# Kernel optimization log

Hardware: AMD Instinct MI355X
Metric: run time of the kernel (lower is better)

Reference implementation:

```python
import jax, jax.numpy as jnp
import numpy as np

HIDDEN = 2048
N_HEADS = 16
N_KV_HEADS = 8
HEAD_DIM = 128  # == head_dim_original, no padding needed
ROPE_THETA = 1000000.0
EPS = 1e-6
T_NOISE = 512
T_CTX = 1536
MAX_KV = 8192


def rms_norm(x, scale, eps=EPS):
    # normalize over last axis (head_dim), per-head like nnx.RMSNorm(head_dim)
    var = jnp.mean(x * x, axis=-1, keepdims=True)
    return x * jax.lax.rsqrt(var + eps) * scale


def apply_rope(x, positions, head_dim=HEAD_DIM, theta=ROPE_THETA):
    # x: (T, N, H), positions: (T,) int
    inv_freq = 1.0 / (theta ** (jnp.arange(0, head_dim, 2, dtype=jnp.float32) / head_dim))
    ang = positions.astype(jnp.float32)[:, None] * inv_freq  # (T, H/2)
    cos = jnp.cos(ang)[:, None, :]  # (T, 1, H/2)
    sin = jnp.sin(ang)[:, None, :]
    x1, x2 = jnp.split(x, 2, axis=-1)
    return jnp.concatenate([x1 * cos - x2 * sin, x2 * cos + x1 * sin], axis=-1).astype(x.dtype)


def setup_inputs() -> dict:
    key = jax.random.key(0)
    ks = jax.random.split(key, 10)
    s = 0.02
    return {
        "x_noise": jax.random.normal(ks[0], (T_NOISE, HIDDEN), jnp.float32),
        "target_hidden": jax.random.normal(ks[1], (T_CTX, HIDDEN), jnp.float32),
        "noise_positions": jnp.arange(T_NOISE, dtype=jnp.int32) + T_CTX,
        "ctx_positions": jnp.arange(T_CTX, dtype=jnp.int32),
        "kv_cache_k": jax.random.normal(ks[2], (1, N_HEADS, MAX_KV, HEAD_DIM), jnp.float32),
        "kv_cache_v": jax.random.normal(ks[3], (1, N_HEADS, MAX_KV, HEAD_DIM), jnp.float32),
        "cache_len": 2048,
        "wq": jax.random.normal(ks[4], (HIDDEN, N_HEADS, HEAD_DIM), jnp.float32) * s,
        "wk": jax.random.normal(ks[5], (HIDDEN, N_KV_HEADS, HEAD_DIM), jnp.float32) * s,
        "wv": jax.random.normal(ks[6], (HIDDEN, N_KV_HEADS, HEAD_DIM), jnp.float32) * s,
        "wo": jax.random.normal(ks[7], (N_HEADS, HEAD_DIM, HIDDEN), jnp.float32) * s,
        "q_scale": jnp.ones((HEAD_DIM,), jnp.float32) + jax.random.uniform(ks[8], (HEAD_DIM,), jnp.float32, -0.05, 0.05),
        "k_scale": jnp.ones((HEAD_DIM,), jnp.float32) + jax.random.uniform(ks[9], (HEAD_DIM,), jnp.float32, -0.05, 0.05),
    }


def reference(x_noise, target_hidden, noise_positions, ctx_positions, kv_cache_k,
              kv_cache_v, cache_len, wq, wk, wv, wo, q_scale, k_scale):
    num_kv_groups = N_HEADS // N_KV_HEADS
    t_noise = x_noise.shape[0]

    # 1. Q projection + RMSNorm + RoPE
    q = jnp.einsum('td,dnh->tnh', x_noise, wq)
    q = rms_norm(q, q_scale)
    q = apply_rope(q, noise_positions)

    # 2. K/V over [context, noise]
    x_new = jnp.concatenate([target_hidden, x_noise], axis=0)  # (T_new, D)
    k_new = jnp.einsum('td,dkh->tkh', x_new, wk)
    v_new = jnp.einsum('td,dkh->tkh', x_new, wv)
    k_new = rms_norm(k_new, k_scale)
    new_positions = jnp.concatenate([ctx_positions, noise_positions], axis=0)
    k_new = apply_rope(k_new, new_positions)

    # 3. GQA head repeat
    if num_kv_groups > 1:
        k_new = jnp.repeat(k_new, num_kv_groups, axis=1)
        v_new = jnp.repeat(v_new, num_kv_groups, axis=1)

    # 4. Scatter new K/V into cache at dynamic offset cache_len
    t_new = x_new.shape[0]
    k_new_4d = k_new.transpose(1, 0, 2)[None]  # (1, N, T_new, H)
    v_new_4d = v_new.transpose(1, 0, 2)[None]
    kv_cache_k = jax.lax.dynamic_update_slice(kv_cache_k, k_new_4d, (0, 0, cache_len, 0))
    kv_cache_v = jax.lax.dynamic_update_slice(kv_cache_v, v_new_4d, (0, 0, cache_len, 0))
    new_cache_len = cache_len + t_new
    max_kv = kv_cache_k.shape[2]

    # 5. Non-causal attention over valid cache (segment-id mask = valid length)
    q_4d = q.transpose(1, 0, 2)[None]  # (1, N, T_noise, H)
    sm_scale = HEAD_DIM ** -0.5
    scores = jnp.einsum('bnth,bnsh->bnts', q_4d, kv_cache_k) * sm_scale  # (1,N,Tq,S)
    valid = jnp.arange(max_kv) < new_cache_len  # (S,)
    scores = jnp.where(valid[None, None, None, :], scores, jnp.float32(-1e30))
    probs = jax.nn.softmax(scores, axis=-1)
    attn = jnp.einsum('bnts,bnsh->bnth', probs, kv_cache_v)
    attn = attn[0].transpose(1, 0, 2)  # (T_noise, N, H)

    output = jnp.einsum('tnh,nhd->td', attn, wo)
    return output, kv_cache_k, kv_cache_v
```

## Files before the change

kernel.cpp:

```cpp
#include <hip/hip_runtime.h>
#include <hip/hip_bf16.h>

#define HIDDEN 2048
#define NH 16
#define NKV 8
#define HD 128
#define TN 512
#define TC 1536
#define TNEW 2048
#define MAXKV 8192

using u16 = unsigned short;
using u32 = unsigned int;

typedef short short8 __attribute__((ext_vector_type(8)));
typedef float floatx4 __attribute__((ext_vector_type(4)));

__device__ __forceinline__ u16 f2bf(float f) {
  u32 u = __float_as_uint(f);
  u += 0x7FFFu + ((u >> 16) & 1u);
  return (u16)(u >> 16);
}

__device__ __forceinline__ uint4 pack8(const float* f) {
  uint4 r;
  r.x = (u32)f2bf(f[0]) | ((u32)f2bf(f[1]) << 16);
  r.y = (u32)f2bf(f[2]) | ((u32)f2bf(f[3]) << 16);
  r.z = (u32)f2bf(f[4]) | ((u32)f2bf(f[5]) << 16);
  r.w = (u32)f2bf(f[6]) | ((u32)f2bf(f[7]) << 16);
  return r;
}

__device__ __forceinline__ short8 ldfrag(const u16* p) {
  uint4 v = *(const uint4*)p;
  return __builtin_bit_cast(short8, v);
}

__device__ __forceinline__ void gload16(const void* g, void* l) {
  __builtin_amdgcn_global_load_lds(
      (const __attribute__((address_space(1))) u32*)g,
      (__attribute__((address_space(3))) u32*)l, 16, 0, 0);
}

__global__ __launch_bounds__(256) void conv_bf16(
    const float4* __restrict__ in, uint2* __restrict__ out, int n4)
{
  int idx = blockIdx.x * 256 + threadIdx.x;
  if (idx >= n4) return;
  float4 v = in[idx];
  uint2 r;
  r.x = (u32)f2bf(v.x) | ((u32)f2bf(v.y) << 16);
  r.y = (u32)f2bf(v.z) | ((u32)f2bf(v.w) << 16);
  out[idx] = r;
}

__global__ __launch_bounds__(256) void transpose_bf16(
    const float* __restrict__ w, u16* __restrict__ wT, int K, int N)
{
  __shared__ float t[64][65];
  const int bk = blockIdx.y * 64, bn = blockIdx.x * 64;
  const int tid = threadIdx.x;
  const int r = tid >> 4, c4 = (tid & 15) * 4;
#pragma unroll
  for (int rr = 0; rr < 4; rr++) {
    float4 v = *(const float4*)(w + (size_t)(bk + rr * 16 + r) * N + bn + c4);
    t[rr * 16 + r][c4 + 0] = v.x;
    t[rr * 16 + r][c4 + 1] = v.y;
    t[rr * 16 + r][c4 + 2] = v.z;
    t[rr * 16 + r][c4 + 3] = v.w;
  }
  __syncthreads();
  const int n = tid >> 2, k16 = (tid & 3) * 16;
  u32 wbuf[8];
#pragma unroll
  for (int jj = 0; jj < 8; jj++) {
    float lo = t[k16 + 2 * jj][n], hi = t[k16 + 2 * jj + 1][n];
    wbuf[jj] = (u32)f2bf(lo) | ((u32)f2bf(hi) << 16);
  }
  *(uint4*)(&wT[(size_t)(bn + n) * K + bk + k16])     = *(uint4*)(wbuf);
  *(uint4*)(&wT[(size_t)(bn + n) * K + bk + k16 + 8]) = *(uint4*)(wbuf + 4);
}

__global__ __launch_bounds__(256) void vT_build(
    const float* __restrict__ inV, const float* __restrict__ vproj,
    const int* __restrict__ clp, u16* __restrict__ VbT)
{
  __shared__ float t[64][65];
  const int cl = *clp;
  const int s0 = blockIdx.x * 64;
  const int slim = cl + TNEW;
  if (s0 >= slim) return;
  const int h0 = blockIdx.y * 64;
  const int head = blockIdx.z;
  const int tid = threadIdx.x;

  const int rr = tid >> 2, c16 = (tid & 3) * 16;
  int s = s0 + rr;
  if (s >= slim) s = slim - 1;
  const float* src = (s < cl)
      ? inV + ((size_t)head * MAXKV + s) * HD + (h0 + c16)
      : vproj + (size_t)(s - cl) * (NKV * HD) + (head >> 1) * HD + (h0 + c16);
  float4 v0 = ((const float4*)src)[0];
  float4 v1 = ((const float4*)src)[1];
  float4 v2 = ((const float4*)src)[2];
  float4 v3 = ((const float4*)src)[3];
  *(float4*)&t[rr][c16 + 0]  = v0;
  *(float4*)&t[rr][c16 + 4]  = v1;
  *(float4*)&t[rr][c16 + 8]  = v2;
  *(float4*)&t[rr][c16 + 12] = v3;
  __syncthreads();

  const int hh = tid >> 2, sseg = (tid & 3) * 16;
  u32 wbuf[8];
#pragma unroll
  for (int j = 0; j < 8; j++)
    wbuf[j] = (u32)f2bf(t[sseg + 2 * j][hh]) | ((u32)f2bf(t[sseg + 2 * j + 1][hh]) << 16);
  u16* dst = VbT + ((size_t)head * HD + h0 + hh) * MAXKV + s0 + sseg;
  *(uint4*)(dst)     = *(uint4*)(wbuf);
  *(uint4*)(dst + 8) = *(uint4*)(wbuf + 4);
}

__global__ __launch_bounds__(256) void cache_copy(
    const float4* __restrict__ inK, const float4* __restrict__ inV,
    float4* __restrict__ outK, float4* __restrict__ outV,
    const int* __restrict__ clp, u16* __restrict__ Kb)
{
  const int cl = *clp;
  long long idx = (long long)blockIdx.x * 256 + threadIdx.x;
  const long long per = (long long)NH * MAXKV * (HD / 4);
  const float4* src; float4* dst; bool isv;
  long long r = idx;
  if (r < per) { src = inK; dst = outK; isv = false; }
  else { r -= per; src = inV; dst = outV; isv = true; }
  int row = (int)((r >> 5) & (MAXKV - 1));
  if (row >= cl && row < cl + TNEW) return;
  float4 v = src[r];
  dst[r] = v;
  if (!isv && row < cl && Kb) {
    uint2 p;
    p.x = (u32)f2bf(v.x) | ((u32)f2bf(v.y) << 16);
    p.y = (u32)f2bf(v.z) | ((u32)f2bf(v.w) << 16);
    *(uint2*)(Kb + (size_t)r * 4) = p;
  }
}

__global__ __launch_bounds__(256) void gemm_v2(
    const u16* __restrict__ A0, int rows0, const u16* __restrict__ A1,
    const u16* __restrict__ B0, const u16* __restrict__ B1, int Nhalf,
    float* __restrict__ C0, float* __restrict__ C1,
    int M, int N, int K, int ksteps)
{
  __shared__ u16 As[2][128 * 32];
  __shared__ u16 Bs[2][128 * 32];
  const int tid = threadIdx.x;
  const int lane = tid & 63, wave = tid >> 6;
  const int quad = lane >> 4, m16 = lane & 15;

  const int gx = gridDim.x, gy = gridDim.y;
  int bx = blockIdx.x, by = blockIdx.y;
  if (((gx & 3) == 0) && ((gy & 1) == 0)) {
    const int lin = bx + gx * by;
    const int c = lin & 7, j = lin >> 3;
    const int sw = gx >> 2, sh = gy >> 1;
    bx = (c & 3) * sw + j % sw;
    by = (c >> 2) * sh + j / sw;
  }
  const int bm = by * 128, bn = bx * 128;
  const int wm = (wave >> 1) * 64, wn = (wave & 1) * 64;
  const int z = blockIdx.z;
  const int kbase = z * ksteps * 32;

  const u16* B = (bn < Nhalf) ? B0 : B1;
  float*     C = (bn < Nhalf) ? C0 : C1;
  const int n0 = (bn < Nhalf) ? bn : bn - Nhalf;
  const int strideN = (bn < Nhalf) ? Nhalf : (N - Nhalf);

  floatx4 acc[4][4];
#pragma unroll
  for (int i = 0; i < 4; i++)
#pragma unroll
    for (int j = 0; j < 4; j++)
#pragma unroll
      for (int r = 0; r < 4; r++) acc[i][j][r] = 0.0f;

  const int srow = tid >> 2;
  const int sk = (tid & 3) * 8;
  const int ar0 = bm + srow, ar1 = bm + srow + 64;
  const u16* Arow0 = (ar0 < rows0) ? (A0 + (size_t)ar0 * K)
                                   : (A1 + (size_t)(ar0 - rows0) * K);
  const u16* Arow1 = (ar1 < rows0) ? (A0 + (size_t)ar1 * K)
                                   : (A1 + (size_t)(ar1 - rows0) * K);
  const u16* Brow0 = B + (size_t)(n0 + srow) * K;
  const u16* Brow1 = B + (size_t)(n0 + srow + 64) * K;
  const int wb = wave * 512;

  {
    const int k0 = kbase;
    gload16(Arow0 + k0 + sk, &As[0][wb]);
    gload16(Arow1 + k0 + sk, &As[0][2048 + wb]);
    gload16(Brow0 + k0 + sk, &Bs[0][wb]);
    gload16(Brow1 + k0 + sk, &Bs[0][2048 + wb]);
  }
  int b = 0;
  for (int ks = 0; ks < ksteps; ks++) {
    if (ks + 1 < ksteps) {
      const int k1 = kbase + (ks + 1) * 32;
      gload16(Arow0 + k1 + sk, &As[b ^ 1][wb]);
      gload16(Arow1 + k1 + sk, &As[b ^ 1][2048 + wb]);
      gload16(Brow0 + k1 + sk, &Bs[b ^ 1][wb]);
      gload16(Brow1 + k1 + sk, &Bs[b ^ 1][2048 + wb]);
      asm volatile("s_waitcnt vmcnt(4)" ::: "memory");
    } else {
      asm volatile("s_waitcnt vmcnt(0)" ::: "memory");
    }
    __builtin_amdgcn_s_barrier();
    __builtin_amdgcn_sched_barrier(0);

    short8 af[4], bfr[4];
#pragma unroll
    for (int i = 0; i < 4; i++) {
      af[i]  = ldfrag(&As[b][(wm + i * 16 + m16) * 32 + quad * 8]);
      bfr[i] = ldfrag(&Bs[b][(wn + i * 16 + m16) * 32 + quad * 8]);
    }
#pragma unroll
    for (int i = 0; i < 4; i++)
#pragma unroll
      for (int j = 0; j < 4; j++)
        acc[i][j] = __builtin_amdgcn_mfma_f32_16x16x32_bf16(af[i], bfr[j], acc[i][j], 0, 0, 0);

    asm volatile("s_waitcnt lgkmcnt(0)" ::: "memory");
    __builtin_amdgcn_s_barrier();
    __builtin_amdgcn_sched_barrier(0);
    b ^= 1;
  }

  const size_t zoff = (size_t)z * M * Nhalf;
#pragma unroll
  for (int i = 0; i < 4; i++)
#pragma unroll
    for (int j = 0; j < 4; j++)
#pragma unroll
      for (int r = 0; r < 4; r++) {
        int row = bm + wm + i * 16 + quad * 4 + r;
        int col = wn + j * 16 + m16;
        C[zoff + (size_t)row * strideN + n0 + col] = acc[i][j][r];
      }
}

__global__ __launch_bounds__(256) void gemm_bf16(
    const float* __restrict__ A0, int rows0, const float* __restrict__ A1,
    const float* __restrict__ B0, const float* __restrict__ B1, int Nhalf,
    float* __restrict__ C0, float* __restrict__ C1,
    int M, int N, int K, int ksteps)
{
  __shared__ u16 As[64 * 40];
  __shared__ u16 Bs[64 * 40];
  const int tid = threadIdx.x;
  const int lane = tid & 63;
  const int wave = tid >> 6;
  const int quad = lane >> 4;
  const int m16 = lane & 15;
  const int bm = blockIdx.y * 64;
  const int bn = blockIdx.x * 64;
  const int wm = (wave >> 1) * 32;
  const int wn = (wave & 1) * 32;
  const int z = blockIdx.z;
  const int kbase = z * ksteps * 32;

  const float* B = (bn < Nhalf) ? B0 : B1;
  float*       C = (bn < Nhalf) ? C0 : C1;
  const int n0 = (bn < Nhalf) ? bn : bn - Nhalf;
  const int strideN = (bn < Nhalf) ? Nhalf : (N - Nhalf);

  floatx4 acc[2][2];
#pragma unroll
  for (int i = 0; i < 2; i++)
#pragma unroll
    for (int j = 0; j < 2; j++)
#pragma unroll
      for (int r = 0; r < 4; r++) acc[i][j][r] = 0.0f;

  const int arow = tid >> 2, akg = (tid & 3) * 8;
  const int brow = tid >> 3, bng = (tid & 7) * 8;
  const int garow = bm + arow;
  const float* Ap = (garow < rows0) ? (A0 + (size_t)garow * K)
                                    : (A1 + (size_t)(garow - rows0) * K);

  for (int ks = 0; ks < ksteps; ks++) {
    const int k0 = kbase + ks * 32;
    if (k0 >= K) break;
    float av[8];
    *(float4*)(av)     = *(const float4*)(Ap + k0 + akg);
    *(float4*)(av + 4) = *(const float4*)(Ap + k0 + akg + 4);
    *(uint4*)&As[arow * 40 + akg] = pack8(av);

    float bv[8];
    const float* Bp = B + (size_t)(k0 + brow) * strideN + n0 + bng;
    *(float4*)(bv)     = *(const float4*)(Bp);
    *(float4*)(bv + 4) = *(const float4*)(Bp + 4);
#pragma unroll
    for (int j = 0; j < 8; j++) Bs[(bng + j) * 40 + brow] = f2bf(bv[j]);

    __syncthreads();

    short8 a0 = ldfrag(&As[(wm + m16) * 40 + quad * 8]);
    short8 a1 = ldfrag(&As[(wm + 16 + m16) * 40 + quad * 8]);
    short8 b0 = ldfrag(&Bs[(wn + m16) * 40 + quad * 8]);
    short8 b1 = ldfrag(&Bs[(wn + 16 + m16) * 40 + quad * 8]);
    acc[0][0] = __builtin_amdgcn_mfma_f32_16x16x32_bf16(a0, b0, acc[0][0], 0, 0, 0);
    acc[0][1] = __builtin_amdgcn_mfma_f32_16x16x32_bf16(a0, b1, acc[0][1], 0, 0, 0);
    acc[1][0] = __builtin_amdgcn_mfma_f32_16x16x32_bf16(a1, b0, acc[1][0], 0, 0, 0);
    acc[1][1] = __builtin_amdgcn_mfma_f32_16x16x32_bf16(a1, b1, acc[1][1], 0, 0, 0);

    __syncthreads();
  }

  const size_t zoff = (size_t)z * M * Nhalf;
#pragma unroll
  for (int mt = 0; mt < 2; mt++)
#pragma unroll
    for (int nt = 0; nt < 2; nt++)
#pragma unroll
      for (int r = 0; r < 4; r++) {
        int row = bm + wm + mt * 16 + quad * 4 + r;
        int col = wn + nt * 16 + m16;
        C[zoff + (size_t)row * strideN + n0 + col] = acc[mt][nt][r];
      }
}

__global__ __launch_bounds__(256) void reduce4(
    const float4* __restrict__ P, float4* __restrict__ C, int n4)
{
  int idx = blockIdx.x * 256 + threadIdx.x;
  if (idx >= n4) return;
  float4 a = P[idx], b = P[idx + n4], c = P[idx + 2 * n4], d = P[idx + 3 * n4];
  float4 r;
  r.x = (a.x + b.x) + (c.x + d.x);
  r.y = (a.y + b.y) + (c.y + d.y);
  r.z = (a.z + b.z) + (c.z + d.z);
  r.w = (a.w + b.w) + (c.w + d.w);
  C[idx] = r;
}

__global__ __launch_bounds__(64) void q_post_k(
    const float* __restrict__ qproj, const int* __restrict__ npos,
    const float* __restrict__ qscale, u16* __restrict__ qbf)
{
  const int t = blockIdx.x, n = blockIdx.y, i = threadIdx.x;
  const size_t base = (size_t)t * HIDDEN + n * HD;
  const float x1 = qproj[base + i];
  const float x2 = qproj[base + i + 64];
  float ss = x1 * x1 + x2 * x2;
#pragma unroll
  for (int m = 1; m < 64; m <<= 1) ss += __shfl_xor(ss, m, 64);
  const float rstd = rsqrtf(ss * (1.0f / HD) + 1e-6f);
  float y1 = x1 * rstd * qscale[i];
  float y2 = x2 * rstd * qscale[i + 64];
  const float pos = (float)npos[t];
  const float ang = pos * exp2f(-(float)i * (19.931568569324174f / 64.0f));
  const float c = cosf(ang), s = sinf(ang);
  const float sc = 0.08838834764831845f * 1.4426950408889634f;
  qbf[base + i]      = f2bf((y1 * c - y2 * s) * sc);
  qbf[base + i + 64] = f2bf((y2 * c + y1 * s) * sc);
}

__global__ __launch_bounds__(64) void k_post_k(
    const float* __restrict__ kproj, const int* __restrict__ ctxpos,
    const int* __restrict__ npos, const float* __restrict__ kscale,
    const int* __restrict__ clp, float* __restrict__ outK, u16* __restrict__ Kb)
{
  const int t = blockIdx.x, kh = blockIdx.y, i = threadIdx.x;
  const int cl = *clp;
  const size_t base = (size_t)t * (NKV * HD) + kh * HD;
  const float x1 = kproj[base + i];
  const float x2 = kproj[base + i + 64];
  float ss = x1 * x1 + x2 * x2;
#pragma unroll
  for (int m = 1; m < 64; m <<= 1) ss += __shfl_xor(ss, m, 64);
  const float rstd = rsqrtf(ss * (1.0f / HD) + 1e-6f);
  float y1 = x1 * rstd * kscale[i];
  float y2 = x2 * rstd * kscale[i + 64];
  const int posi = (t < TC) ? ctxpos[t] : npos[t - TC];
  const float ang = (float)posi * exp2f(-(float)i * (19.931568569324174f / 64.0f));
  const float c = cosf(ang), s = sinf(ang);
  const float o1 = y1 * c - y2 * s;
  const float o2 = y2 * c + y1 * s;
  const size_t row = (size_t)cl + t;
  const size_t b0 = ((size_t)(2 * kh) * MAXKV + row) * HD;
  const size_t b1 = ((size_t)(2 * kh + 1) * MAXKV + row) * HD;
  outK[b0 + i] = o1; outK[b0 + i + 64] = o2;
  outK[b1 + i] = o1; outK[b1 + i + 64] = o2;
  if (Kb) {
    const u16 s1 = f2bf(o1), s2 = f2bf(o2);
    Kb[b0 + i] = s1; Kb[b0 + i + 64] = s2;
    Kb[b1 + i] = s1; Kb[b1 + i + 64] = s2;
  }
}

__global__ __launch_bounds__(128) void v_post_k(
    const float* __restrict__ vproj, const int* __restrict__ clp,
    float* __restrict__ outV)
{
  const int t = blockIdx.x, kh = blockIdx.y, h = threadIdx.x;
  const int cl = *clp;
  const float v = vproj[(size_t)t * (NKV * HD) + kh * HD + h];
  const size_t row = (size_t)cl + t;
  outV[((size_t)(2 * kh) * MAXKV + row) * HD + h] = v;
  outV[((size_t)(2 * kh + 1) * MAXKV + row) * HD + h] = v;
}

__global__ __launch_bounds__(256) void attn_sh(
    const u16* __restrict__ qbf, const u16* __restrict__ Kb,
    const u16* __restrict__ VbT, const int* __restrict__ clp,
    float* __restrict__ Opart, float* __restrict__ Oml, int splits)
{
  __shared__ u16 Ks[2][32 * 128];
  __shared__ u16 Vt[2][128 * 32];
  __shared__ u16 Ps[4][16 * 40];

  const int tid = threadIdx.x;
  const int lane = tid & 63, wave = tid >> 6;
  const int quad = lane >> 4, m16 = lane & 15;

  const int lin = blockIdx.x;
  const int ppx = (NH * splits) >> 3;
  const int c = lin & 7;
  const int jj = lin >> 3;
  const int pair = c * ppx + (jj % ppx);
  const int x = jj / ppx;
  const int head = pair & (NH - 1);
  const int z = pair >> 4;

  const int qbase = x * 64 + wave * 16;
  const int Svalid = *clp + TNEW;
  const int ntiles = (Svalid + 31) >> 5;
  const int per = (ntiles + splits - 1) / splits;
  const int it0 = z * per;
  const int it1 = (ntiles < it0 + per) ? ntiles : (it0 + per);

  short8 qf[4];
#pragma unroll
  for (int kb = 0; kb < 4; kb++)
    qf[kb] = ldfrag(&qbf[((size_t)(qbase + m16) * NH + head) * HD + kb * 32 + quad * 8]);

  floatx4 O[8];
#pragma unroll
  for (int i = 0; i < 8; i++)
#pragma unroll
    for (int r = 0; r < 4; r++) O[i][r] = 0.0f;
  float lrow[4];
#pragma unroll
  for (int r = 0; r < 4; r++) lrow[r] = 0.0f;

  const int krow = tid >> 4;
  const int ksrccol = ((tid & 15) * 16) ^ ((krow & 7) << 4);
  const char* Kbase = (const char*)(Kb + (size_t)head * MAXKV * HD);
  const int vh = tid >> 2;
  const int vs8 = (tid & 3) * 8;
  const char* Vbase = (const char*)(VbT + (size_t)head * HD * MAXKV);
  u16* myPs = &Ps[wave][0];
  const int kxor = (m16 & 7) << 4;
  const int wb = wave * 512;

  int b = 0;
  if (it0 < it1) {
    {
      const int s0 = it0 * 32;
      gload16(Kbase + ((size_t)(s0 + krow) << 8) + ksrccol,          &Ks[0][wb]);
      gload16(Kbase + ((size_t)(s0 + krow + 16) << 8) + ksrccol,     &Ks[0][2048 + wb]);
      gload16(Vbase + (((size_t)vh * MAXKV + s0 + vs8) << 1),        &Vt[0][wb]);
      gload16(Vbase + (((size_t)(vh + 64) * MAXKV + s0 + vs8) << 1), &Vt[0][2048 + wb]);
    }
    for (int it = it0; it < it1; ++it) {
      if (it + 1 < it1) {
        const int s1 = (it + 1) * 32;
        u16* KsN = &Ks[b ^ 1][0];
        u16* VtN = &Vt[b ^ 1][0];
        gload16(Kbase + ((size_t)(s1 + krow) << 8) + ksrccol,          KsN + wb);
        gload16(Kbase + ((size_t)(s1 + krow + 16) << 8) + ksrccol,     KsN + 2048 + wb);
        gload16(Vbase + (((size_t)vh * MAXKV + s1 + vs8) << 1),        VtN + wb);
        gload16(Vbase + (((size_t)(vh + 64) * MAXKV + s1 + vs8) << 1), VtN + 2048 + wb);
        asm volatile("s_waitcnt vmcnt(4) lgkmcnt(0)" ::: "memory");
      } else {
        asm volatile("s_waitcnt vmcnt(0) lgkmcnt(0)" ::: "memory");
      }
      __builtin_amdgcn_s_barrier();
      __builtin_amdgcn_sched_barrier(0);

      const u16* KsB = &Ks[b][0];
      const u16* VtB = &Vt[b][0];
      const int s0 = it * 32;

      floatx4 sc[2];
#pragma unroll
      for (int st = 0; st < 2; st++) {
        floatx4 a;
#pragma unroll
        for (int r = 0; r < 4; r++) a[r] = 0.0f;
        const int rofs = (st * 16 + m16) * 128;
#pragma unroll
        for (int kb = 0; kb < 4; kb++) {
          short8 kf = ldfrag(&KsB[rofs + (((kb * 64 + quad * 16) ^ kxor) >> 1)]);
          a = __builtin_amdgcn_mfma_f32_16x16x32_bf16(qf[kb], kf, a, 0, 0, 0);
        }
        const int scol = s0 + st * 16 + m16;
        if (scol >= Svalid) {
#pragma unroll
          for (int r = 0; r < 4; r++) a[r] = -1e30f;
        }
        sc[st] = a;
      }

#pragma unroll
      for (int st = 0; st < 2; st++)
#pragma unroll
        for (int r = 0; r < 4; r++) sc[st][r] = exp2f(sc[st][r]);
#pragma unroll
      for (int r = 0; r < 4; r++) lrow[r] += sc[0][r] + sc[1][r];

#pragma unroll
      for (int st = 0; st < 2; st++)
#pragma unroll
        for (int r = 0; r < 4; r++)
          myPs[(quad * 4 + r) * 40 + st * 16 + m16] = f2bf(sc[st][r]);
      short8 pfr = ldfrag(&myPs[m16 * 40 + quad * 8]);
#pragma unroll
      for (int hb = 0; hb < 8; hb++) {
        short8 vf = ldfrag(&VtB[(hb * 16 + m16) * 32 + quad * 8]);
        O[hb] = __builtin_amdgcn_mfma_f32_16x16x32_bf16(pfr, vf, O[hb], 0, 0, 0);
      }

      asm volatile("s_waitcnt lgkmcnt(0)" ::: "memory");
      __builtin_amdgcn_s_barrier();
      __builtin_amdgcn_sched_barrier(0);
      b ^= 1;
    }
  }

#pragma unroll
  for (int r = 0; r < 4; r++) {
    lrow[r] += __shfl_xor(lrow[r], 1, 64);
    lrow[r] += __shfl_xor(lrow[r], 2, 64);
    lrow[r] += __shfl_xor(lrow[r], 4, 64);
    lrow[r] += __shfl_xor(lrow[r], 8, 64);
  }

  const size_t zbase = (size_t)z * TN * NH;
  const int trow = qbase + quad * 4;
#pragma unroll
  for (int hb = 0; hb < 8; hb++)
#pragma unroll
    for (int r = 0; r < 4; r++)
      Opart[(zbase + (size_t)(trow + r) * NH + head) * HD + hb * 16 + m16] = O[hb][r];
  if (m16 == 0) {
#pragma unroll
    for (int r = 0; r < 4; r++) {
      Oml[(zbase + (size_t)(trow + r) * NH + head) * 2 + 0] = 0.0f;
      Oml[(zbase + (size_t)(trow + r) * NH + head) * 2 + 1] = lrow[r];
    }
  }
}

__global__ __launch_bounds__(256) void attn_k(
    const u16* __restrict__ qbf, const float* __restrict__ outK,
    const float* __restrict__ outV, const int* __restrict__ clp,
    float* __restrict__ Opart, float* __restrict__ Oml)
{
  __shared__ u16 Ksl[32 * 136];
  __shared__ u16 Vtl[128 * 40];
  __shared__ u16 Psl[4 * 16 * 40];
  const int tid = threadIdx.x;
  const int lane = tid & 63, wave = tid >> 6;
  const int quad = lane >> 4, m16 = lane & 15;
  const int head = blockIdx.y;
  const int qbase = blockIdx.x * 64 + wave * 16;
  const int z = blockIdx.z, splits = gridDim.z;
  const int Svalid = *clp + TNEW;
  const int ntiles = (Svalid + 31) >> 5;
  const int per = (ntiles + splits - 1) / splits;
  const int it0 = z * per;
  const int it1 = min(ntiles, it0 + per);

  short8 qf[4];
#pragma unroll
  for (int kb = 0; kb < 4; kb++)
    qf[kb] = ldfrag(&qbf[((size_t)(qbase + m16) * NH + head) * HD + kb * 32 + quad * 8]);

  floatx4 O[8];
#pragma unroll
  for (int i = 0; i < 8; i++)
#pragma unroll
    for (int r = 0; r < 4; r++) O[i][r] = 0.0f;
  float mrow[4], lrow[4];
#pragma unroll
  for (int r = 0; r < 4; r++) { mrow[r] = -1e30f; lrow[r] = 0.0f; }

  const int sstage = tid >> 3;
  const int hg = (tid & 7) * 16;

  for (int it = it0; it < it1; it++) {
    const int s0 = it * 32;
    {
      int srow = s0 + sstage; if (srow > MAXKV - 1) srow = MAXKV - 1;
      const float* kp = outK + ((size_t)head * MAXKV + srow) * HD + hg;
      float tv[16];
      *(float4*)(tv)      = *(const float4*)(kp);
      *(float4*)(tv + 4)  = *(const float4*)(kp + 4);
      *(float4*)(tv + 8)  = *(const float4*)(kp + 8);
      *(float4*)(tv + 12) = *(const float4*)(kp + 12);
      *(uint4*)&Ksl[sstage * 136 + hg]     = pack8(tv);
      *(uint4*)&Ksl[sstage * 136 + hg + 8] = pack8(tv + 8);
      const float* vp = outV + ((size_t)head * MAXKV + srow) * HD + hg;
      float vv[16];
      *(float4*)(vv)      = *(const float4*)(vp);
      *(float4*)(vv + 4)  = *(const float4*)(vp + 4);
      *(float4*)(vv + 8)  = *(const float4*)(vp + 8);
      *(float4*)(vv + 12) = *(const float4*)(vp + 12);
#pragma unroll
      for (int j = 0; j < 16; j++) Vtl[(hg + j) * 40 + sstage] = f2bf(vv[j]);
    }
    __syncthreads();

    floatx4 sc[2];
#pragma unroll
    for (int st = 0; st < 2; st++) {
      floatx4 a;
#pragma unroll
      for (int r = 0; r < 4; r++) a[r] = 0.0f;
#pragma unroll
      for (int kb = 0; kb < 4; kb++) {
        short8 kf = ldfrag(&Ksl[(st * 16 + m16) * 136 + kb * 32 + quad * 8]);
        a = __builtin_amdgcn_mfma_f32_16x16x32_bf16(qf[kb], kf, a, 0, 0, 0);
      }
      const int scol = s0 + st * 16 + m16;
      if (scol >= Svalid) {
#pragma unroll
        for (int r = 0; r < 4; r++) a[r] = -1e30f;
      }
      sc[st] = a;
    }

    float alpha[4];
#pragma unroll
    for (int r = 0; r < 4; r++) {
      float mx = fmaxf(sc[0][r], sc[1][r]);
      mx = fmaxf(mx, __shfl_xor(mx, 1, 64));
      mx = fmaxf(mx, __shfl_xor(mx, 2, 64));
      mx = fmaxf(mx, __shfl_xor(mx, 4, 64));
      mx = fmaxf(mx, __shfl_xor(mx, 8, 64));
      const float mn = fmaxf(mrow[r], mx);
      alpha[r] = exp2f(mrow[r] - mn);
      const float p0 = exp2f(sc[0][r] - mn);
      const float p1 = exp2f(sc[1][r] - mn);
      sc[0][r] = p0; sc[1][r] = p1;
      float rs = p0 + p1;
      rs += __shfl_xor(rs, 1, 64);
      rs += __shfl_xor(rs, 2, 64);
      rs += __shfl_xor(rs, 4, 64);
      rs += __shfl_xor(rs, 8, 64);
      lrow[r] = lrow[r] * alpha[r] + rs;
      mrow[r] = mn;
    }
#pragma unroll
    for (int hb = 0; hb < 8; hb++)
#pragma unroll
      for (int r = 0; r < 4; r++) O[hb][r] *= alpha[r];

    u16* myPs = &Psl[wave * 640];
#pragma unroll
    for (int st = 0; st < 2; st++)
#pragma unroll
      for (int r = 0; r < 4; r++)
        myPs[(quad * 4 + r) * 40 + st * 16 + m16] = f2bf(sc[st][r]);
    short8 pf = ldfrag(&myPs[m16 * 40 + quad * 8]);
#pragma unroll
    for (int hb = 0; hb < 8; hb++) {
      short8 vf = ldfrag(&Vtl[(hb * 16 + m16) * 40 + quad * 8]);
      O[hb] = __builtin_amdgcn_mfma_f32_16x16x32_bf16(pf, vf, O[hb], 0, 0, 0);
    }
    __syncthreads();
  }

  const size_t zbase = (size_t)z * TN * NH;
  const int trow = qbase + quad * 4;
#pragma unroll
  for (int hb = 0; hb < 8; hb++)
#pragma unroll
    for (int r = 0; r < 4; r++)
      Opart[(zbase + (size_t)(trow + r) * NH + head) * HD + hb * 16 + m16] = O[hb][r];
  if (m16 == 0) {
#pragma unroll
    for (int r = 0; r < 4; r++) {
      Oml[(zbase + (size_t)(trow + r) * NH + head) * 2 + 0] = mrow[r];
      Oml[(zbase + (size_t)(trow + r) * NH + head) * 2 + 1] = lrow[r];
    }
  }
}

__global__ __launch_bounds__(128) void attn_combine(
    const float* __restrict__ Opart, const float* __restrict__ Oml,
    float* __restrict__ attnb, u16* __restrict__ attnbf, int splits)
{
  const int pair = blockIdx.x;
  const int h = threadIdx.x;
  float M = -1e30f;
  for (int zz = 0; zz < splits; zz++)
    M = fmaxf(M, Oml[((size_t)zz * TN * NH + pair) * 2]);
  float l = 0.0f, o = 0.0f;
  for (int zz = 0; zz < splits; zz++) {
    const float mi = Oml[((size_t)zz * TN * NH + pair) * 2];
    const float li = Oml[((size_t)zz * TN * NH + pair) * 2 + 1];
    const float w = exp2f(mi - M);
    l += li * w;
    o += Opart[((size_t)zz * TN * NH + pair) * HD + h] * w;
  }
  const float res = o / l;
  attnb[(size_t)pair * HD + h] = res;
  if (attnbf) attnbf[(size_t)pair * HD + h] = f2bf(res);
}

extern "C" void kernel_launch(void* const* d_in, const int* in_sizes, int n_in,
                              void* d_out, int out_size, void* d_ws, size_t ws_size,
                              hipStream_t stream) {
  const float* x_noise       = (const float*)d_in[0];
  const float* target_hidden = (const float*)d_in[1];
  const int*   noise_pos     = (const int*)d_in[2];
  const int*   ctx_pos       = (const int*)d_in[3];
  const float* inK           = (const float*)d_in[4];
  const float* inV           = (const float*)d_in[5];
  const int*   cache_len     = (const int*)d_in[6];
  const float* wq            = (const float*)d_in[7];
  const float* wk            = (const float*)d_in[8];
  const float* wv            = (const float*)d_in[9];
  const float* wo            = (const float*)d_in[10];
  const float* q_scale       = (const float*)d_in[11];
  const float* k_scale       = (const float*)d_in[12];

  float* out0 = (float*)d_out;
  float* outK = out0 + (size_t)TN * HIDDEN;
  float* outV = outK + (size_t)NH * MAXKV * HD;

  size_t off = 0;
  auto walloc = [&](size_t bytes) -> void* {
    void* p = (char*)d_ws + off;
    off += (bytes + 255) & ~(size_t)255;
    return p;
  };
  u16*   qbf    = (u16*)walloc((size_t)TN * HIDDEN * 2);
  float* attnb  = (float*)walloc((size_t)TN * HIDDEN * 4);
  u16*   attnbf = (u16*)walloc((size_t)TN * HIDDEN * 2);
  float* qproj  = (float*)walloc((size_t)TN * HIDDEN * 4);
  float* kproj  = (float*)walloc((size_t)TNEW * NKV * HD * 4);
  float* vproj  = (float*)walloc((size_t)TNEW * NKV * HD * 4);

  const size_t PER_SPLIT = (size_t)TN * NH * HD * 4 + (size_t)TN * NH * 8;
  const size_t SHB   = (size_t)NH * MAXKV * HD * sizeof(u16);
  const size_t GPART = (size_t)4 * TN * HIDDEN * 4;
  const size_t CONVB = ((size_t)TN * HIDDEN + (size_t)TC * HIDDEN) * 2
                     + ((size_t)HIDDEN * HIDDEN * 2
                      + (size_t)HIDDEN * (NKV * HD) * 2) * 2;
  auto maxsz = [](size_t a, size_t b) { return a > b ? a : b; };

  size_t avail = (ws_size > off) ? ws_size - off : 0;
  bool conv = false;
  int asplits = 0;
  if (avail >= CONVB + 2 * SHB + maxsz(8 * PER_SPLIT, GPART))      { conv = true; asplits = 8; }
  else if (avail >= CONVB + 2 * SHB + maxsz(4 * PER_SPLIT, GPART)) { conv = true; asplits = 4; }
  else if (avail >= 2 * SHB + maxsz(8 * PER_SPLIT, GPART))         { asplits = 8; }
  else if (avail >= 2 * SHB + maxsz(4 * PER_SPLIT, GPART))         { asplits = 4; }
  const bool shadow = (asplits > 0);

  u16 *xbf = nullptr, *thbf = nullptr, *wqT = nullptr, *wkT = nullptr,
      *wvT = nullptr, *woT = nullptr;
  if (conv) {
    xbf  = (u16*)walloc((size_t)TN * HIDDEN * 2);
    thbf = (u16*)walloc((size_t)TC * HIDDEN * 2);
    wqT  = (u16*)walloc((size_t)HIDDEN * HIDDEN * 2);
    wkT  = (u16*)walloc((size_t)HIDDEN * (NKV * HD) * 2);
    wvT  = (u16*)walloc((size_t)HIDDEN * (NKV * HD) * 2);
    woT  = (u16*)walloc((size_t)HIDDEN * HIDDEN * 2);
  }
  u16 *Kb = nullptr, *VbT = nullptr;
  if (shadow) {
    Kb  = (u16*)walloc(SHB);
    VbT = (u16*)walloc(SHB);
  }

  float* scratch = (float*)((char*)d_ws + off);
  const size_t avail2 = (ws_size > off) ? ws_size - off : 0;
  if (!shadow) {
    asplits = 2;
    if (avail2 >= 8 * PER_SPLIT) asplits = 8;
    else if (avail2 >= 4 * PER_SPLIT) asplits = 4;
  }
  float* Opart = scratch;
  float* Oml   = Opart + (size_t)asplits * TN * NH * HD;
  const bool ksplit = (avail2 >= GPART);
  float* gpart = scratch;

  if (conv) {
    conv_bf16<<<dim3((TN * HIDDEN / 4 + 255) / 256), dim3(256), 0, stream>>>(
        (const float4*)x_noise, (uint2*)xbf, TN * HIDDEN / 4);
    conv_bf16<<<dim3((TC * HIDDEN / 4 + 255) / 256), dim3(256), 0, stream>>>(
        (const float4*)target_hidden, (uint2*)thbf, TC * HIDDEN / 4);
    transpose_bf16<<<dim3(HIDDEN / 64, HIDDEN / 64), dim3(256), 0, stream>>>(
        wq, wqT, HIDDEN, HIDDEN);
    transpose_bf16<<<dim3(NKV * HD / 64, HIDDEN / 64), dim3(256), 0, stream>>>(
        wk, wkT, HIDDEN, NKV * HD);
    transpose_bf16<<<dim3(NKV * HD / 64, HIDDEN / 64), dim3(256), 0, stream>>>(
        wv, wvT, HIDDEN, NKV * HD);
    transpose_bf16<<<dim3(HIDDEN / 64, HIDDEN / 64), dim3(256), 0, stream>>>(
        wo, woT, NH * HD, HIDDEN);
  }

  cache_copy<<<dim3(32768), dim3(256), 0, stream>>>(
      (const float4*)inK, (const float4*)inV, (float4*)outK, (float4*)outV,
      cache_len, Kb);

  if (conv && ksplit) {
    gemm_v2<<<dim3(HIDDEN / 128, TN / 128, 4), dim3(256), 0, stream>>>(
        xbf, TN, xbf, wqT, wqT, HIDDEN, gpart, gpart, TN, HIDDEN, HIDDEN, 16);
    reduce4<<<dim3((TN * HIDDEN / 4 + 255) / 256), dim3(256), 0, stream>>>(
        (const float4*)gpart, (float4*)qproj, TN * HIDDEN / 4);
  } else if (conv) {
    gemm_v2<<<dim3(HIDDEN / 128, TN / 128, 1), dim3(256), 0, stream>>>(
        xbf, TN, xbf, wqT, wqT, HIDDEN, qproj, qproj, TN, HIDDEN, HIDDEN, 64);
  } else if (ksplit) {
    gemm_bf16<<<dim3(HIDDEN / 64, TN / 64, 4), dim3(256), 0, stream>>>(
        x_noise, TN, x_noise, wq, wq, HIDDEN, gpart, gpart, TN, HIDDEN, HIDDEN, 16);
    reduce4<<<dim3((TN * HIDDEN / 4 + 255) / 256), dim3(256), 0, stream>>>(
        (const float4*)gpart, (float4*)qproj, TN * HIDDEN / 4);
  } else {
    gemm_bf16<<<dim3(HIDDEN / 64, TN / 64, 1), dim3(256), 0, stream>>>(
        x_noise, TN, x_noise, wq, wq, HIDDEN, qproj, qproj, TN, HIDDEN, HIDDEN, 64);
  }

  if (conv) {
    gemm_v2<<<dim3(2 * NKV * HD / 128, TNEW / 128, 1), dim3(256), 0, stream>>>(
        thbf, TC, xbf, wkT, wvT, NKV * HD, kproj, vproj,
        TNEW, 2 * NKV * HD, HIDDEN, 64);
  } else {
    gemm_bf16<<<dim3(2 * NKV * HD / 64, TNEW / 64, 1), dim3(256), 0, stream>>>(
        target_hidden, TC, x_noise, wk, wv, NKV * HD, kproj, vproj,
        TNEW, 2 * NKV * HD, HIDDEN, 64);
  }

  q_post_k<<<dim3(TN, NH), dim3(64), 0, stream>>>(qproj, noise_pos, q_scale, qbf);
  k_post_k<<<dim3(TNEW, NKV), dim3(64), 0, stream>>>(
      kproj, ctx_pos, noise_pos, k_scale, cache_len, outK, Kb);
  v_post_k<<<dim3(TNEW, NKV), dim3(128), 0, stream>>>(vproj, cache_len, outV);
  if (shadow) {
    vT_build<<<dim3(MAXKV / 64, HD / 64, NH), dim3(256), 0, stream>>>(
        inV, vproj, cache_len, VbT);
  }

  if (shadow) {
    attn_sh<<<dim3((TN / 64) * NH * asplits), dim3(256), 0, stream>>>(
        qbf, Kb, VbT, cache_len, Opart, Oml, asplits);
  } else {
    attn_k<<<dim3(TN / 64, NH, asplits), dim3(256), 0, stream>>>(
        qbf, outK, outV, cache_len, Opart, Oml);
  }
  attn_combine<<<dim3(TN * NH), dim3(128), 0, stream>>>(
      Opart, Oml, attnb, conv ? attnbf : nullptr, asplits);

  if (conv && ksplit) {
    gemm_v2<<<dim3(HIDDEN / 128, TN / 128, 4), dim3(256), 0, stream>>>(
        attnbf, TN, attnbf, woT, woT, HIDDEN, gpart, gpart, TN, HIDDEN, HIDDEN, 16);
    reduce4<<<dim3((TN * HIDDEN / 4 + 255) / 256), dim3(256), 0, stream>>>(
        (const float4*)gpart, (float4*)out0, TN * HIDDEN / 4);
  } else if (conv) {
    gemm_v2<<<dim3(HIDDEN / 128, TN / 128, 1), dim3(256), 0, stream>>>(
        attnbf, TN, attnbf, woT, woT, HIDDEN, out0, out0, TN, HIDDEN, HIDDEN, 64);
  } else if (ksplit) {
    gemm_bf16<<<dim3(HIDDEN / 64, TN / 64, 4), dim3(256), 0, stream>>>(
        attnb, TN, attnb, wo, wo, HIDDEN, gpart, gpart, TN, HIDDEN, HIDDEN, 16);
    reduce4<<<dim3((TN * HIDDEN / 4 + 255) / 256), dim3(256), 0, stream>>>(
        (const float4*)gpart, (float4*)out0, TN * HIDDEN / 4);
  } else {
    gemm_bf16<<<dim3(HIDDEN / 64, TN / 64, 1), dim3(256), 0, stream>>>(
        attnb, TN, attnb, wo, wo, HIDDEN, out0, out0, TN, HIDDEN, HIDDEN, 64);
  }
}
```

Measured before the change: 469.7 us.

## Shrink gemm_v2 M tile to 64 and XOR-swizzle LDS fragments

The gemm_v2 block tile goes from 128x128 to 64x128, so each wave computes 32x64 and the grids double along M. This gives more blocks for the small GEMMs. It also applies an XOR swizzle to the K column within the 32-wide LDS rows for the A/B tiles in gemm_v2 and for the V tile in the attention kernel, to reduce LDS bank conflicts on fragment reads. The cost is lower arithmetic intensity per block and more global traffic for B.

```diff
diff --git a/kernel.cpp b/kernel.cpp
--- a/kernel.cpp
+++ b/kernel.cpp
@@ -150,7 +150,7 @@
     float* __restrict__ C0, float* __restrict__ C1,
     int M, int N, int K, int ksteps)
 {
-  __shared__ u16 As[2][128 * 32];
+  __shared__ u16 As[2][64 * 32];
   __shared__ u16 Bs[2][128 * 32];
   const int tid = threadIdx.x;
   const int lane = tid & 63, wave = tid >> 6;
@@ -165,8 +165,8 @@
     bx = (c & 3) * sw + j % sw;
     by = (c >> 2) * sh + j / sw;
   }
-  const int bm = by * 128, bn = bx * 128;
-  const int wm = (wave >> 1) * 64, wn = (wave & 1) * 64;
+  const int bm = by * 64, bn = bx * 128;
+  const int wm = (wave >> 1) * 32, wn = (wave & 1) * 64;
   const int z = blockIdx.z;
   const int kbase = z * ksteps * 32;
 
@@ -175,55 +175,53 @@
   const int n0 = (bn < Nhalf) ? bn : bn - Nhalf;
   const int strideN = (bn < Nhalf) ? Nhalf : (N - Nhalf);
 
-  floatx4 acc[4][4];
-#pragma unroll
-  for (int i = 0; i < 4; i++)
+  floatx4 acc[2][4];
+#pragma unroll
+  for (int i = 0; i < 2; i++)
 #pragma unroll
     for (int j = 0; j < 4; j++)
 #pragma unroll
       for (int r = 0; r < 4; r++) acc[i][j][r] = 0.0f;
 
   const int srow = tid >> 2;
-  const int sk = (tid & 3) * 8;
-  const int ar0 = bm + srow, ar1 = bm + srow + 64;
-  const u16* Arow0 = (ar0 < rows0) ? (A0 + (size_t)ar0 * K)
-                                   : (A1 + (size_t)(ar0 - rows0) * K);
-  const u16* Arow1 = (ar1 < rows0) ? (A0 + (size_t)ar1 * K)
-                                   : (A1 + (size_t)(ar1 - rows0) * K);
+  const int sk = ((tid & 3) * 8) ^ (((srow >> 1) & 3) << 3);
+  const int ar = bm + srow;
+  const u16* Arow = (ar < rows0) ? (A0 + (size_t)ar * K)
+                                 : (A1 + (size_t)(ar - rows0) * K);
   const u16* Brow0 = B + (size_t)(n0 + srow) * K;
   const u16* Brow1 = B + (size_t)(n0 + srow + 64) * K;
   const int wb = wave * 512;
 
   {
     const int k0 = kbase;
-    gload16(Arow0 + k0 + sk, &As[0][wb]);
-    gload16(Arow1 + k0 + sk, &As[0][2048 + wb]);
+    gload16(Arow  + k0 + sk, &As[0][wb]);
     gload16(Brow0 + k0 + sk, &Bs[0][wb]);
     gload16(Brow1 + k0 + sk, &Bs[0][2048 + wb]);
   }
+  const int rq = (quad * 8) ^ (((m16 >> 1) & 3) << 3);
   int b = 0;
   for (int ks = 0; ks < ksteps; ks++) {
     if (ks + 1 < ksteps) {
       const int k1 = kbase + (ks + 1) * 32;
-      gload16(Arow0 + k1 + sk, &As[b ^ 1][wb]);
-      gload16(Arow1 + k1 + sk, &As[b ^ 1][2048 + wb]);
+      gload16(Arow  + k1 + sk, &As[b ^ 1][wb]);
       gload16(Brow0 + k1 + sk, &Bs[b ^ 1][wb]);
       gload16(Brow1 + k1 + sk, &Bs[b ^ 1][2048 + wb]);
-      asm volatile("s_waitcnt vmcnt(4)" ::: "memory");
+      asm volatile("s_waitcnt vmcnt(3)" ::: "memory");
     } else {
       asm volatile("s_waitcnt vmcnt(0)" ::: "memory");
     }
     __builtin_amdgcn_s_barrier();
     __builtin_amdgcn_sched_barrier(0);
 
-    short8 af[4], bfr[4];
-#pragma unroll
-    for (int i = 0; i < 4; i++) {
-      af[i]  = ldfrag(&As[b][(wm + i * 16 + m16) * 32 + quad * 8]);
-      bfr[i] = ldfrag(&Bs[b][(wn + i * 16 + m16) * 32 + quad * 8]);
-    }
-#pragma unroll
-    for (int i = 0; i < 4; i++)
+    short8 af[2], bfr[4];
+#pragma unroll
+    for (int i = 0; i < 2; i++)
+      af[i] = ldfrag(&As[b][(wm + i * 16 + m16) * 32 + rq]);
+#pragma unroll
+    for (int j = 0; j < 4; j++)
+      bfr[j] = ldfrag(&Bs[b][(wn + j * 16 + m16) * 32 + rq]);
+#pragma unroll
+    for (int i = 0; i < 2; i++)
 #pragma unroll
       for (int j = 0; j < 4; j++)
         acc[i][j] = __builtin_amdgcn_mfma_f32_16x16x32_bf16(af[i], bfr[j], acc[i][j], 0, 0, 0);
@@ -236,7 +234,7 @@
 
   const size_t zoff = (size_t)z * M * Nhalf;
 #pragma unroll
-  for (int i = 0; i < 4; i++)
+  for (int i = 0; i < 2; i++)
 #pragma unroll
     for (int j = 0; j < 4; j++)
 #pragma unroll
@@ -456,10 +454,11 @@
   const int ksrccol = ((tid & 15) * 16) ^ ((krow & 7) << 4);
   const char* Kbase = (const char*)(Kb + (size_t)head * MAXKV * HD);
   const int vh = tid >> 2;
-  const int vs8 = (tid & 3) * 8;
+  const int vs8 = ((tid & 3) * 8) ^ (((vh >> 1) & 3) << 3);
   const char* Vbase = (const char*)(VbT + (size_t)head * HD * MAXKV);
   u16* myPs = &Ps[wave][0];
   const int kxor = (m16 & 7) << 4;
+  const int vq = (quad * 8) ^ (((m16 >> 1) & 3) << 3);
   const int wb = wave * 512;
 
   int b = 0;
@@ -526,7 +525,7 @@
       short8 pfr = ldfrag(&myPs[m16 * 40 + quad * 8]);
 #pragma unroll
       for (int hb = 0; hb < 8; hb++) {
-        short8 vf = ldfrag(&VtB[(hb * 16 + m16) * 32 + quad * 8]);
+        short8 vf = ldfrag(&VtB[(hb * 16 + m16) * 32 + vq]);
         O[hb] = __builtin_amdgcn_mfma_f32_16x16x32_bf16(pfr, vf, O[hb], 0, 0, 0);
       }
 
@@ -818,12 +817,12 @@
       cache_len, Kb);
 
   if (conv && ksplit) {
-    gemm_v2<<<dim3(HIDDEN / 128, TN / 128, 4), dim3(256), 0, stream>>>(
+    gemm_v2<<<dim3(HIDDEN / 128, TN / 64, 4), dim3(256), 0, stream>>>(
         xbf, TN, xbf, wqT, wqT, HIDDEN, gpart, gpart, TN, HIDDEN, HIDDEN, 16);
     reduce4<<<dim3((TN * HIDDEN / 4 + 255) / 256), dim3(256), 0, stream>>>(
         (const float4*)gpart, (float4*)qproj, TN * HIDDEN / 4);
   } else if (conv) {
-    gemm_v2<<<dim3(HIDDEN / 128, TN / 128, 1), dim3(256), 0, stream>>>(
+    gemm_v2<<<dim3(HIDDEN / 128, TN / 64, 1), dim3(256), 0, stream>>>(
         xbf, TN, xbf, wqT, wqT, HIDDEN, qproj, qproj, TN, HIDDEN, HIDDEN, 64);
   } else if (ksplit) {
     gemm_bf16<<<dim3(HIDDEN / 64, TN / 64, 4), dim3(256), 0, stream>>>(
@@ -836,7 +835,7 @@
   }
 
   if (conv) {
-    gemm_v2<<<dim3(2 * NKV * HD / 128, TNEW / 128, 1), dim3(256), 0, stream>>>(
+    gemm_v2<<<dim3(2 * NKV * HD / 128, TNEW / 64, 1), dim3(256), 0, stream>>>(
         thbf, TC, xbf, wkT, wvT, NKV * HD, kproj, vproj,
         TNEW, 2 * NKV * HD, HIDDEN, 64);
   } else {
@@ -865,12 +864,12 @@
       Opart, Oml, attnb, conv ? attnbf : nullptr, asplits);
 
   if (conv && ksplit) {
-    gemm_v2<<<dim3(HIDDEN / 128, TN / 128, 4), dim3(256), 0, stream>>>(
+    gemm_v2<<<dim3(HIDDEN / 128, TN / 64, 4), dim3(256), 0, stream>>>(
         attnbf, TN, attnbf, woT, woT, HIDDEN, gpart, gpart, TN, HIDDEN, HIDDEN, 16);
     reduce4<<<dim3((TN * HIDDEN / 4 + 255) / 256), dim3(256), 0, stream>>>(
         (const float4*)gpart, (float4*)out0, TN * HIDDEN / 4);
   } else if (conv) {
-    gemm_v2<<<dim3(HIDDEN / 128, TN / 128, 1), dim3(256), 0, stream>>>(
+    gemm_v2<<<dim3(HIDDEN / 128, TN / 64, 1), dim3(256), 0, stream>>>(
         attnbf, TN, attnbf, woT, woT, HIDDEN, out0, out0, TN, HIDDEN, HIDDEN, 64);
   } else if (ksplit) {
     gemm_bf16<<<dim3(HIDDEN / 64, TN / 64, 4), dim3(256), 0, stream>>>(
```

After: 459.4 us. 1.02x faster.
